# Kernel optimization log

Hardware: AMD Instinct MI355X
Metric: run time of the kernel (lower is better)

## Reference

```python
import jax, jax.numpy as jnp
import numpy as np

N_EMBD = 1024
N_HEAD = 16
HEAD_DIM = N_EMBD // N_HEAD


def setup_inputs() -> dict:
    key = jax.random.key(0)
    ks = jax.random.split(key, 5)
    B, T, C = 2, 2048, N_EMBD
    scale = 0.02
    return {
        "x": jax.random.normal(ks[0], (B, T, C), dtype=jnp.float32),
        "w_attn": jax.random.normal(ks[1], (C, 3 * C), dtype=jnp.float32) * scale,
        "b_attn": jax.random.normal(ks[2], (3 * C,), dtype=jnp.float32) * scale,
        "w_proj": jax.random.normal(ks[3], (C, C), dtype=jnp.float32) * scale,
        "b_proj": jax.random.normal(ks[4], (C,), dtype=jnp.float32) * scale,
    }


def reference(x, w_attn, b_attn, w_proj, b_proj):
    B, T, C = x.shape
    H, D = N_HEAD, HEAD_DIM
    qkv = x @ w_attn + b_attn  # [B,T,3C]
    q, k, v = jnp.split(qkv, 3, axis=-1)
    # [B,T,C] -> [B,H,T,D]
    q = q.reshape(B, T, H, D).transpose(0, 2, 1, 3)
    k = k.reshape(B, T, H, D).transpose(0, 2, 1, 3)
    v = v.reshape(B, T, H, D).transpose(0, 2, 1, 3)
    scores = jnp.einsum("bhqd,bhkd->bhqk", q, k) / jnp.sqrt(jnp.float32(D))
    causal = jnp.tril(jnp.ones((T, T), dtype=bool))
    scores = jnp.where(causal, scores, jnp.finfo(scores.dtype).min)
    attn = jax.nn.softmax(scores, axis=-1)
    y = jnp.einsum("bhqk,bhkd->bhqd", attn, v)  # [B,H,T,D]
    y = y.transpose(0, 2, 1, 3).reshape(B, T, C)
    return y @ w_proj + b_proj
```

## Files before the change

kernel.cpp:

```cpp
#include <hip/hip_runtime.h>

typedef unsigned short u16;
typedef u16 u16x4 __attribute__((ext_vector_type(4)));
typedef u16 u16x8 __attribute__((ext_vector_type(8)));
typedef __bf16 bf16x8 __attribute__((ext_vector_type(8)));
typedef float floatx4 __attribute__((ext_vector_type(4)));

#define N_EMBD 1024
#define N_HEAD 16
#define HEAD_DIM 64
#define SEQ 2048
#define BATCH 2
#define M_ROWS (BATCH * SEQ)

typedef __attribute__((address_space(1))) const unsigned char ga_t;
typedef __attribute__((address_space(3))) unsigned char la_t;

#if __has_builtin(__builtin_amdgcn_exp2f)
#define EXP2(x) __builtin_amdgcn_exp2f(x)
#else
#define EXP2(x) exp2f(x)
#endif

__device__ __forceinline__ u16 cvt_bf16(float f) {
  return __builtin_bit_cast(u16, (__bf16)f);
}

__global__ __launch_bounds__(256) void prep(const float* __restrict__ x,
                                            u16* __restrict__ xb,
                                            const float* __restrict__ wa,
                                            const float* __restrict__ wp,
                                            u16* __restrict__ outa,
                                            u16* __restrict__ outp) {
  const int bid = blockIdx.x;
  if (bid < 2048) {
    const long i = ((long)bid * 256 + threadIdx.x) * 8;
    const float4 f0 = *(const float4*)&x[i];
    const float4 f1 = *(const float4*)&x[i + 4];
    u16x8 p;
    p[0] = cvt_bf16(f0.x); p[1] = cvt_bf16(f0.y);
    p[2] = cvt_bf16(f0.z); p[3] = cvt_bf16(f0.w);
    p[4] = cvt_bf16(f1.x); p[5] = cvt_bf16(f1.y);
    p[6] = cvt_bf16(f1.z); p[7] = cvt_bf16(f1.w);
    *(u16x8*)&xb[i] = p;
    return;
  }
  __shared__ u16 tile[32][33];
  const int t = bid - 2048;
  const int gx = t & 127;
  const int gy = t >> 7;
  const int R = N_EMBD;
  const float* in;
  u16* out;
  int C, bx;
  if (gx < 96) {
    in = wa; out = outa; C = 3 * N_EMBD; bx = gx * 32;
  } else {
    in = wp; out = outp; C = N_EMBD; bx = (gx - 96) * 32;
  }
  const int by = gy * 32;
  const int tx = threadIdx.x & 31;
  const int ty = threadIdx.x >> 5;
#pragma unroll
  for (int j = 0; j < 32; j += 8)
    tile[ty + j][tx] = cvt_bf16(in[(long)(by + ty + j) * C + bx + tx]);
  __syncthreads();
#pragma unroll
  for (int j = 0; j < 32; j += 8)
    out[(long)(bx + ty + j) * R + by + tx] = tile[tx][ty + j];
}

#define BK 32

template <int MODE>
__device__ __forceinline__ void stage128(const u16* __restrict__ A,
                                         const u16* __restrict__ Bt, int bm,
                                         int bn, int kt, int K, int tid,
                                         u16* as, u16* bs) {
  const int w = tid >> 6;
  const int l = tid & 63;
  const int lrow = l >> 2;
#pragma unroll
  for (int p = 0; p < 2; ++p) {
    const int arow = p * 64 + w * 16;
    const int row = arow + lrow;
    const int sl = (l & 3) ^ ((row >> 1) & 3);
    long gA;
    if (MODE == 0) {
      gA = (long)(bm + row) * K + kt + sl * 8;
    } else {
      const int m = bm + row;
      const int b = m >> 11, t = m & 2047;
      const int k0 = kt + sl * 8;
      const int head = k0 >> 6, dd = k0 & 63;
      gA = (((long)(b * N_HEAD + head)) * SEQ + t) * HEAD_DIM + dd;
    }
    __builtin_amdgcn_global_load_lds((ga_t*)(A + gA), (la_t*)&as[arow * BK],
                                     16, 0, 0);
  }
  constexpr int TN = (MODE == 1) ? 64 : 128;
#pragma unroll
  for (int p = 0; p < TN / 64; ++p) {
    const int arow = p * 64 + w * 16;
    const int row = arow + lrow;
    const int sl = (l & 3) ^ ((row >> 1) & 3);
    const long gB = (long)(bn + row) * K + kt + sl * 8;
    __builtin_amdgcn_global_load_lds((ga_t*)(Bt + gB), (la_t*)&bs[arow * BK],
                                     16, 0, 0);
  }
}

template <int MODE>
__global__ __launch_bounds__(256) void gemm128(
    const u16* __restrict__ A, const u16* __restrict__ Bt,
    const float* __restrict__ bias, float* __restrict__ out,
    u16* __restrict__ qo, u16* __restrict__ ko, u16* __restrict__ vo, int N,
    int K) {
  constexpr int TN = (MODE == 1) ? 64 : 128;
  constexpr int NJ = TN / 32;
  __shared__ u16 As[3][128 * BK];
  __shared__ u16 Bs[3][TN * BK];
  const int tid = threadIdx.x;

  const int nx = gridDim.x;
  const int nwg = nx * gridDim.y;
  int lin = blockIdx.y * nx + blockIdx.x;
  lin = (lin & 7) * (nwg >> 3) + (lin >> 3);
  const int bm = (lin / nx) * 128;
  const int bn = (lin % nx) * TN;

  const int w = tid >> 6;
  const int l = tid & 63;
  const int wm = (w >> 1) * 64;
  const int wn = (w & 1) * (TN / 2);
  const int m16 = l & 15;
  const int quad = l >> 4;
  const int ksw = (quad ^ ((m16 >> 1) & 3)) * 8;

  floatx4 acc[4][NJ];
#pragma unroll
  for (int i = 0; i < 4; ++i)
#pragma unroll
    for (int j = 0; j < NJ; ++j) acc[i][j] = (floatx4){0.f, 0.f, 0.f, 0.f};

  const int nk = K / BK;
  stage128<MODE>(A, Bt, bm, bn, 0, K, tid, As[0], Bs[0]);
  stage128<MODE>(A, Bt, bm, bn, BK, K, tid, As[1], Bs[1]);

  u16 *a0 = As[0], *a1 = As[1], *a2 = As[2];
  u16 *b0 = Bs[0], *b1 = Bs[1], *b2 = Bs[2];

  for (int t = 0; t < nk; ++t) {
    if (t + 1 < nk) {
      if constexpr (MODE == 0)
        asm volatile("s_waitcnt vmcnt(4)" ::: "memory");
      else
        asm volatile("s_waitcnt vmcnt(3)" ::: "memory");
    } else {
      asm volatile("s_waitcnt vmcnt(0)" ::: "memory");
    }
    __builtin_amdgcn_s_barrier();

    if (t + 2 < nk)
      stage128<MODE>(A, Bt, bm, bn, (t + 2) * BK, K, tid, a2, b2);

    bf16x8 af[4], bfr[NJ];
#pragma unroll
    for (int i = 0; i < 4; ++i)
      af[i] = __builtin_bit_cast(
          bf16x8, *(const u16x8*)&a0[(wm + i * 16 + m16) * BK + ksw]);
#pragma unroll
    for (int j = 0; j < NJ; ++j)
      bfr[j] = __builtin_bit_cast(
          bf16x8, *(const u16x8*)&b0[(wn + j * 16 + m16) * BK + ksw]);
#pragma unroll
    for (int i = 0; i < 4; ++i)
#pragma unroll
      for (int j = 0; j < NJ; ++j)
        acc[i][j] = __builtin_amdgcn_mfma_f32_16x16x32_bf16(af[i], bfr[j],
                                                            acc[i][j], 0, 0, 0);
    u16* ta = a0; a0 = a1; a1 = a2; a2 = ta;
    u16* tb = b0; b0 = b1; b1 = b2; b2 = tb;
  }

#pragma unroll
  for (int i = 0; i < 4; ++i) {
#pragma unroll
    for (int j = 0; j < NJ; ++j) {
      const int col = bn + wn + j * 16 + m16;
      const float bv = bias[col];
      if (MODE == 1) {
#pragma unroll
        for (int r = 0; r < 4; ++r) {
          const int row = bm + wm + i * 16 + quad * 4 + r;
          out[(long)row * N_EMBD + col] = acc[i][j][r] + bv;
        }
      } else {
        const int which = col >> 10;
        const int cc = col & 1023;
        const int h = cc >> 6;
        const int dd = cc & 63;
        const int row0 = bm + wm + i * 16 + quad * 4;
        const int b = row0 >> 11;
        const int t0 = row0 & 2047;
        if (which == 2) {
          u16x4 pk;
#pragma unroll
          for (int r = 0; r < 4; ++r) pk[r] = cvt_bf16(acc[i][j][r] + bv);
          *(u16x4*)&vo[(((long)(b * N_HEAD + h)) * HEAD_DIM + dd) * SEQ + t0] =
              pk;
        } else {
          u16* dst = (which == 0) ? qo : ko;
#pragma unroll
          for (int r = 0; r < 4; ++r)
            dst[(((long)(b * N_HEAD + h)) * SEQ + t0 + r) * HEAD_DIM + dd] =
                cvt_bf16(acc[i][j][r] + bv);
        }
      }
    }
  }
}

#define BQ 64
#define BKV 64
#define LOG2E 1.44269504f
#define NQT (SEQ / BQ)
#define NROWS (32 * SEQ)

__device__ __forceinline__ void stage_kv(const u16* __restrict__ K,
                                         const u16* __restrict__ Vt, long bh,
                                         int kt, int tid, u16* kl, u16* vl) {
#pragma unroll
  for (int i = 0; i < 2; ++i) {
    const int p = tid + 256 * i;
    const int row = p >> 3;
    const int slot = (p & 7) ^ (row & 7);
    const int wb = (i * 256 + (tid & 192)) * 8;
    __builtin_amdgcn_global_load_lds(
        (ga_t*)&K[(bh * SEQ + kt + row) * HEAD_DIM + slot * 8], (la_t*)&kl[wb],
        16, 0, 0);
    __builtin_amdgcn_global_load_lds(
        (ga_t*)&Vt[(bh * HEAD_DIM + row) * SEQ + kt + slot * 8], (la_t*)&vl[wb],
        16, 0, 0);
  }
}

__global__ __launch_bounds__(256, 4) void flash_attn(
    const u16* __restrict__ Qy, const u16* __restrict__ K,
    const u16* __restrict__ Vt, float* __restrict__ Opart,
    float2* __restrict__ mlpart) {
  const int id = blockIdx.x;
  const int a = id >> 6;
  const int h = (id >> 5) & 1;
  const long bh = id & 31;
  const int tid = threadIdx.x;
  const int w = tid >> 6;
  const int l = tid & 63;
  const int m16 = l & 15;
  const int quad = l >> 4;

  __shared__ u16 Kl[2][BKV * 64];
  __shared__ u16 Vl[2][64 * BKV];
  __shared__ u16 Pl[4][16 * 64];

  const float SC = 0.125f * LOG2E;
  const int sw = (m16 & 7) << 3;

  for (int ph = 0; ph < 2; ++ph) {
    const int iq = ph ? (31 - a) : a;
    const int na = iq + 1;
    const int mid = (na + 1) >> 1;
    const int s0 = h ? mid : 0;
    const int e0 = h ? na : mid;
    const int qglob = iq * BQ + w * 16 + m16;

    bf16x8 qf[2];
    {
      const u16* qrow = Qy + (bh * SEQ + qglob) * HEAD_DIM;
      qf[0] = __builtin_bit_cast(bf16x8, *(const u16x8*)&qrow[quad * 8]);
      qf[1] = __builtin_bit_cast(bf16x8, *(const u16x8*)&qrow[32 + quad * 8]);
    }

    floatx4 Oacc[4];
#pragma unroll
    for (int t = 0; t < 4; ++t) Oacc[t] = (floatx4){0.f, 0.f, 0.f, 0.f};
    float mrow = -1e30f, lsum = 0.f;

    if (s0 < e0) {
      stage_kv(K, Vt, bh, s0 * BKV, tid, Kl[0], Vl[0]);
      __syncthreads();

      for (int it = s0; it < e0; ++it) {
        const int buf = (it - s0) & 1;
        const int kt = it * BKV;
        if (it + 1 < e0)
          stage_kv(K, Vt, bh, kt + BKV, tid, Kl[buf ^ 1], Vl[buf ^ 1]);

        floatx4 s[4];
#pragma unroll
        for (int j = 0; j < 4; ++j) s[j] = (floatx4){0.f, 0.f, 0.f, 0.f};
        __builtin_amdgcn_s_setprio(1);
#pragma unroll
        for (int j = 0; j < 4; ++j)
#pragma unroll
          for (int kk = 0; kk < 2; ++kk) {
            const bf16x8 kf = __builtin_bit_cast(
                bf16x8, *(const u16x8*)&Kl[buf][(j * 16 + m16) * 64 +
                                                ((kk * 32 + quad * 8) ^ sw)]);
            s[j] = __builtin_amdgcn_mfma_f32_16x16x32_bf16(kf, qf[kk], s[j], 0,
                                                           0, 0);
          }
        __builtin_amdgcn_s_setprio(0);
        if (it == na - 1) {
#pragma unroll
          for (int j = 0; j < 4; ++j) {
            const int key0 = kt + j * 16 + quad * 4;
#pragma unroll
            for (int r = 0; r < 4; ++r)
              if (key0 + r > qglob) s[j][r] = -1e30f;
          }
        }

        float tm = s[0][0];
#pragma unroll
        for (int j = 0; j < 4; ++j)
#pragma unroll
          for (int r = 0; r < 4; ++r)
            if (j + r) tm = fmaxf(tm, s[j][r]);
        tm = fmaxf(tm, __shfl_xor(tm, 16, 64));
        tm = fmaxf(tm, __shfl_xor(tm, 32, 64));
        const float pm = tm * SC;
        if (!__all(pm <= mrow + 4.f)) {
          const float mn = fmaxf(mrow, pm);
          const float al = EXP2(mrow - mn);
          mrow = mn;
          lsum *= al;
#pragma unroll
          for (int t = 0; t < 4; ++t)
#pragma unroll
            for (int r = 0; r < 4; ++r) Oacc[t][r] *= al;
        }

        float ls = 0.f;
#pragma unroll
        for (int j = 0; j < 4; ++j) {
          u16x4 pk;
#pragma unroll
          for (int r = 0; r < 4; ++r) {
            const float p = EXP2(__builtin_fmaf(s[j][r], SC, -mrow));
            ls += p;
            pk[r] = cvt_bf16(p);
          }
          *(u16x4*)&Pl[w][m16 * 64 + ((j * 16 + quad * 4) ^ sw)] = pk;
        }
        lsum += ls;

        bf16x8 pf[2];
        pf[0] = __builtin_bit_cast(
            bf16x8, *(const u16x8*)&Pl[w][m16 * 64 + ((quad * 8) ^ sw)]);
        pf[1] = __builtin_bit_cast(
            bf16x8, *(const u16x8*)&Pl[w][m16 * 64 + ((32 + quad * 8) ^ sw)]);
        __builtin_amdgcn_s_setprio(1);
#pragma unroll
        for (int t = 0; t < 4; ++t)
#pragma unroll
          for (int kk = 0; kk < 2; ++kk) {
            const bf16x8 vf = __builtin_bit_cast(
                bf16x8, *(const u16x8*)&Vl[buf][(t * 16 + m16) * 64 +
                                                ((kk * 32 + quad * 8) ^ sw)]);
            Oacc[t] = __builtin_amdgcn_mfma_f32_16x16x32_bf16(vf, pf[kk],
                                                              Oacc[t], 0, 0, 0);
          }
        __builtin_amdgcn_s_setprio(0);
        __syncthreads();
      }
    }

    float lt = lsum;
    lt += __shfl_xor(lt, 16, 64);
    lt += __shfl_xor(lt, 32, 64);
    const long row = bh * SEQ + qglob;
    float* Op = Opart + (long)h * NROWS * HEAD_DIM;
#pragma unroll
    for (int t = 0; t < 4; ++t)
      *(floatx4*)&Op[row * HEAD_DIM + t * 16 + quad * 4] = Oacc[t];
    if (quad == 0) mlpart[h * NROWS + row] = make_float2(mrow, lt);
  }
}

__global__ __launch_bounds__(256) void merge_attn(
    const float* __restrict__ Opart, const float2* __restrict__ mlpart,
    u16* __restrict__ Qy) {
  const int bid = blockIdx.x;
  const int bh = (bid & 7) | (((bid >> 10) & 3) << 3);
  const int chunk = (bid >> 3) & 127;
  const int r = threadIdx.x >> 4;
  const int d0 = (threadIdx.x & 15) * 4;
  const long row = (long)bh * SEQ + chunk * 16 + r;
  const float2 A = mlpart[row];
  const float2 B = mlpart[NROWS + row];
  const float M = fmaxf(A.x, B.x);
  const float w0 = EXP2(A.x - M), w1 = EXP2(B.x - M);
  const float inv = 1.f / (w0 * A.y + w1 * B.y);
  const floatx4 o0 = *(const floatx4*)&Opart[row * HEAD_DIM + d0];
  const floatx4 o1 =
      *(const floatx4*)&Opart[(long)NROWS * HEAD_DIM + row * HEAD_DIM + d0];
  u16x4 pk;
#pragma unroll
  for (int i = 0; i < 4; ++i)
    pk[i] = cvt_bf16((w0 * o0[i] + w1 * o1[i]) * inv);
  *(u16x4*)&Qy[row * HEAD_DIM + d0] = pk;
}

extern "C" void kernel_launch(void* const* d_in, const int* in_sizes, int n_in,
                              void* d_out, int out_size, void* d_ws,
                              size_t ws_size, hipStream_t stream) {
  const float* x = (const float*)d_in[0];
  const float* w_attn = (const float*)d_in[1];
  const float* b_attn = (const float*)d_in[2];
  const float* w_proj = (const float*)d_in[3];
  const float* b_proj = (const float*)d_in[4];
  float* out = (float*)d_out;

  char* ws = (char*)d_ws;
  const size_t SZ = (size_t)BATCH * N_HEAD * SEQ * HEAD_DIM * sizeof(u16);
  u16* q = (u16*)(ws);
  u16* k = (u16*)(ws + SZ);
  u16* vT = (u16*)(ws + 2 * SZ);
  u16* wT_a = (u16*)(ws + 3 * SZ);
  u16* wT_p = (u16*)(ws + 3 * SZ + (size_t)3 * N_EMBD * N_EMBD * sizeof(u16));
  u16* xb = (u16*)(ws + 3 * SZ + (size_t)4 * N_EMBD * N_EMBD * sizeof(u16));
  float* Opart = (float*)(ws + (size_t)48 * 1024 * 1024);
  float2* mlpart =
      (float2*)(ws + (size_t)48 * 1024 * 1024 +
                (size_t)2 * NROWS * HEAD_DIM * sizeof(float));

  prep<<<2048 + 4096, 256, 0, stream>>>(x, xb, w_attn, w_proj, wT_a, wT_p);

  gemm128<0><<<dim3(3 * N_EMBD / 128, M_ROWS / 128), 256, 0, stream>>>(
      xb, wT_a, b_attn, nullptr, q, k, vT, 3 * N_EMBD, N_EMBD);

  flash_attn<<<1024, 256, 0, stream>>>(q, k, vT, Opart, mlpart);

  merge_attn<<<4096, 256, 0, stream>>>(Opart, mlpart, q);

  gemm128<1><<<dim3(N_EMBD / 64, M_ROWS / 128), 256, 0, stream>>>(
      q, wT_p, b_proj, out, nullptr, nullptr, nullptr, N_EMBD, N_EMBD);
}
```

Before: 178.5 us.

## Replace QKV GEMM with 256x256-tile 512-thread kernel using direct LDS loads

Adds a new gemm256 kernel for the QKV projection. It uses 256x256 output tiles, 512 threads, BK=64 with double-buffered global_load_lds staging into XOR-swizzled shared memory, and an XCD-aware block remap. The larger tiles raise arithmetic intensity and data reuse per block. The grid shrinks to 192 blocks and each block needs 128KB of LDS, which cuts occupancy and can leave part of the 256 CUs idle.

```diff
diff --git a/kernel.cpp b/kernel.cpp
--- a/kernel.cpp
+++ b/kernel.cpp
@@ -70,6 +70,134 @@
     out[(long)(bx + ty + j) * R + by + tx] = tile[tx][ty + j];
 }
 
+#define GBK 64
+
+__device__ __forceinline__ void stage256(const u16* __restrict__ A,
+                                         const u16* __restrict__ Bt, int bm,
+                                         int bn, int kt, int tid, u16* as,
+                                         u16* bs) {
+#pragma unroll
+  for (int i = 0; i < 4; ++i) {
+    const int p = tid + 512 * i;
+    const int row = p >> 3;
+    const int sl = (p & 7) ^ (row & 7);
+    const int wb = (i * 512 + (tid & 448)) * 8;
+    __builtin_amdgcn_global_load_lds(
+        (ga_t*)&A[(long)(bm + row) * N_EMBD + kt + sl * 8], (la_t*)&as[wb], 16,
+        0, 0);
+    __builtin_amdgcn_global_load_lds(
+        (ga_t*)&Bt[(long)(bn + row) * N_EMBD + kt + sl * 8], (la_t*)&bs[wb], 16,
+        0, 0);
+  }
+}
+
+__global__ __launch_bounds__(512) void gemm256(
+    const u16* __restrict__ A, const u16* __restrict__ Bt,
+    const float* __restrict__ bias, u16* __restrict__ qo, u16* __restrict__ ko,
+    u16* __restrict__ vo) {
+  extern __shared__ u16 smem[];
+  u16* As = smem;
+  u16* Bs = smem + 2 * 256 * 64;
+  const int tid = threadIdx.x;
+
+  const int nx = gridDim.x;
+  const int nwg = nx * gridDim.y;
+  int lin = blockIdx.y * nx + blockIdx.x;
+  lin = (lin & 7) * (nwg >> 3) + (lin >> 3);
+  const int bm = (lin / nx) * 256;
+  const int bn = (lin % nx) * 256;
+
+  const int w = tid >> 6;
+  const int l = tid & 63;
+  const int wm = (w >> 2) * 128;
+  const int wn = (w & 3) * 64;
+  const int m16 = l & 15;
+  const int quad = l >> 4;
+  const int rsw = m16 & 7;
+
+  floatx4 acc[8][4];
+#pragma unroll
+  for (int i = 0; i < 8; ++i)
+#pragma unroll
+    for (int j = 0; j < 4; ++j) acc[i][j] = (floatx4){0.f, 0.f, 0.f, 0.f};
+
+  stage256(A, Bt, bm, bn, 0, tid, As, Bs);
+  stage256(A, Bt, bm, bn, GBK, tid, As + 256 * 64, Bs + 256 * 64);
+  asm volatile("s_waitcnt vmcnt(8)" ::: "memory");
+  __builtin_amdgcn_s_barrier();
+
+  for (int kt = 0; kt < 16; ++kt) {
+    u16* as = As + (kt & 1) * (256 * 64);
+    u16* bs = Bs + (kt & 1) * (256 * 64);
+
+    bf16x8 af[8][2], bf[4][2];
+#pragma unroll
+    for (int i = 0; i < 8; ++i)
+#pragma unroll
+      for (int kk = 0; kk < 2; ++kk)
+        af[i][kk] = __builtin_bit_cast(
+            bf16x8, *(const u16x8*)&as[(wm + i * 16 + m16) * 64 +
+                                       (((kk * 4 + quad) ^ rsw) * 8)]);
+#pragma unroll
+    for (int j = 0; j < 4; ++j)
+#pragma unroll
+      for (int kk = 0; kk < 2; ++kk)
+        bf[j][kk] = __builtin_bit_cast(
+            bf16x8, *(const u16x8*)&bs[(wn + j * 16 + m16) * 64 +
+                                       (((kk * 4 + quad) ^ rsw) * 8)]);
+    asm volatile("s_waitcnt lgkmcnt(0)" ::: "memory");
+    __builtin_amdgcn_s_barrier();
+
+    if (kt + 2 < 16) {
+      stage256(A, Bt, bm, bn, (kt + 2) * GBK, tid, as, bs);
+      asm volatile("s_waitcnt vmcnt(8)" ::: "memory");
+    } else {
+      asm volatile("s_waitcnt vmcnt(0)" ::: "memory");
+    }
+    __builtin_amdgcn_s_barrier();
+
+    __builtin_amdgcn_s_setprio(1);
+#pragma unroll
+    for (int kk = 0; kk < 2; ++kk)
+#pragma unroll
+      for (int i = 0; i < 8; ++i)
+#pragma unroll
+        for (int j = 0; j < 4; ++j)
+          acc[i][j] = __builtin_amdgcn_mfma_f32_16x16x32_bf16(
+              af[i][kk], bf[j][kk], acc[i][j], 0, 0, 0);
+    __builtin_amdgcn_s_setprio(0);
+  }
+
+#pragma unroll
+  for (int i = 0; i < 8; ++i) {
+#pragma unroll
+    for (int j = 0; j < 4; ++j) {
+      const int col = bn + wn + j * 16 + m16;
+      const float bv = bias[col];
+      const int which = col >> 10;
+      const int cc = col & 1023;
+      const int h = cc >> 6;
+      const int dd = cc & 63;
+      const int row0 = bm + wm + i * 16 + quad * 4;
+      const int b = row0 >> 11;
+      const int t0 = row0 & 2047;
+      if (which == 2) {
+        u16x4 pk;
+#pragma unroll
+        for (int r = 0; r < 4; ++r) pk[r] = cvt_bf16(acc[i][j][r] + bv);
+        *(u16x4*)&vo[(((long)(b * N_HEAD + h)) * HEAD_DIM + dd) * SEQ + t0] =
+            pk;
+      } else {
+        u16* dst = (which == 0) ? qo : ko;
+#pragma unroll
+        for (int r = 0; r < 4; ++r)
+          dst[(((long)(b * N_HEAD + h)) * SEQ + t0 + r) * HEAD_DIM + dd] =
+              cvt_bf16(acc[i][j][r] + bv);
+      }
+    }
+  }
+}
+
 #define BK 32
 
 template <int MODE>
@@ -437,8 +565,8 @@
 
   prep<<<2048 + 4096, 256, 0, stream>>>(x, xb, w_attn, w_proj, wT_a, wT_p);
 
-  gemm128<0><<<dim3(3 * N_EMBD / 128, M_ROWS / 128), 256, 0, stream>>>(
-      xb, wT_a, b_attn, nullptr, q, k, vT, 3 * N_EMBD, N_EMBD);
+  gemm256<<<dim3(3 * N_EMBD / 256, M_ROWS / 256), 512, 128 * 1024, stream>>>(
+      xb, wT_a, b_attn, q, k, vT);
 
   flash_attn<<<1024, 256, 0, stream>>>(q, k, vT, Opart, mlpart);
 
```

Result: no change. 181.9 us (+1.9%).
